# Optimization experiments

Hardware: AMD Instinct MI355X
Metric: run time of the kernel (lower is better)

Reference implementation:

```python
import jax, jax.numpy as jnp
import numpy as np

N = 32768      # total nodes per batched graph
E = 262144     # edges per batched graph (avg in-degree 8)
B = 64         # number of graphs in the batch (for mean_nodes readout)
DIN = 20
H = 512
BN_EPS = 1e-5


def setup_inputs() -> dict:
    key = jax.random.key(0)
    ks = jax.random.split(key, 24)
    p = lambda k, shape: jax.random.normal(k, shape, jnp.float32) * 0.02
    inp = {
        "x1": jax.random.normal(ks[0], (N, DIN), jnp.float32),
        "x2": jax.random.normal(ks[1], (N, DIN), jnp.float32),
        "src1": jax.random.randint(ks[2], (E,), 0, N, jnp.int32),
        "dst1": jax.random.randint(ks[3], (E,), 0, N, jnp.int32),
        "src2": jax.random.randint(ks[4], (E,), 0, N, jnp.int32),
        "dst2": jax.random.randint(ks[5], (E,), 0, N, jnp.int32),
        "gids1": jnp.repeat(jnp.arange(B, dtype=jnp.int32), N // B),
        "gids2": jnp.repeat(jnp.arange(B, dtype=jnp.int32), N // B),
        # shared parameters (applied to both graphs, as in the torch module)
        "W_init": p(ks[6], (DIN, H)), "b_init": jnp.zeros((H,), jnp.float32),
        "W1": p(ks[7], (H, H)), "b1": jnp.zeros((H,), jnp.float32),
        "W2": p(ks[8], (H, H)), "b2": jnp.zeros((H,), jnp.float32),
        "gamma1": jnp.ones((H,), jnp.float32), "beta1": jnp.zeros((H,), jnp.float32),
        "gamma2": jnp.ones((H,), jnp.float32), "beta2": jnp.zeros((H,), jnp.float32),
        "Wfc": p(ks[9], (2 * H, 256)), "bfc": jnp.zeros((256,), jnp.float32),
        "Wfc2": p(ks[10], (256, 1)), "bfc2": jnp.zeros((1,), jnp.float32),
    }
    return inp


def _bn_relu(z, gamma, beta):
    # BatchNorm1d in training mode: biased batch stats over the node axis
    mu = jnp.mean(z, axis=0)
    var = jnp.var(z, axis=0)
    return jax.nn.relu(gamma * (z - mu) * jax.lax.rsqrt(var + BN_EPS) + beta)


def _gin_mean(h, src, dst, W, b):
    # DGL GINConv(apply=Linear, aggregator='mean', eps=0):
    # out = Linear(h + mean_{j in N_in(v)} h_j); isolated nodes get 0 agg.
    msg_sum = jax.ops.segment_sum(h[src], dst, num_segments=N)      # [N,H]
    deg = jax.ops.segment_sum(jnp.ones((src.shape[0],), h.dtype), dst, num_segments=N)
    agg = msg_sum / jnp.maximum(deg, 1.0)[:, None]
    return (h + agg) @ W + b


def _encode(x, src, dst, gids, W_init, b_init, W1, b1, W2, b2,
            gamma1, beta1, gamma2, beta2):
    h0 = x @ W_init + b_init
    h1 = _bn_relu(_gin_mean(h0, src, dst, W1, b1), gamma1, beta1)
    h2 = _bn_relu(_gin_mean(h1, src, dst, W2, b2), gamma2, beta2)
    # dgl.mean_nodes: per-graph mean over nodes
    s = jax.ops.segment_sum(h2, gids, num_segments=B)               # [B,H]
    cnt = jax.ops.segment_sum(jnp.ones((h2.shape[0],), h2.dtype), gids, num_segments=B)
    return s / jnp.maximum(cnt, 1.0)[:, None]


def reference(x1, x2, src1, dst1, src2, dst2, gids1, gids2,
              W_init, b_init, W1, b1, W2, b2,
              gamma1, beta1, gamma2, beta2, Wfc, bfc, Wfc2, bfc2):
    g1_emb = _encode(x1, src1, dst1, gids1, W_init, b_init, W1, b1, W2, b2,
                     gamma1, beta1, gamma2, beta2)
    g2_emb = _encode(x2, src2, dst2, gids2, W_init, b_init, W1, b1, W2, b2,
                     gamma1, beta1, gamma2, beta2)
    x = jnp.concatenate([g1_emb, g2_emb], axis=1)                   # [B,2H]
    x = jax.nn.relu(x @ Wfc + bfc)
    return jax.nn.sigmoid(x @ Wfc2 + bfc2)                          # [B,1]
```

## Files before the change

kernel.cpp:

```cpp
#include <hip/hip_runtime.h>
#include <hip/hip_bf16.h>
#include <cstdint>

#define NN 32768
#define EE 262144
#define MM 65536
#define HH 512
#define BB 64
#define DIN 20
#define BN_EPS 1e-5f

__device__ __forceinline__ float bflo(uint32_t w) { return __builtin_bit_cast(float, w << 16); }
__device__ __forceinline__ float bfhi(uint32_t w) { return __builtin_bit_cast(float, w & 0xffff0000u); }
__device__ __forceinline__ uint32_t f2bf_u(float f) {
  uint32_t u = __builtin_bit_cast(uint32_t, f);
  return (u + 0x7fffu + ((u >> 16) & 1u)) >> 16;
}
__device__ __forceinline__ uint32_t pack2(float lo, float hi) {
  return f2bf_u(lo) | (f2bf_u(hi) << 16);
}

typedef float f32x4 __attribute__((ext_vector_type(4)));
typedef float f32x2 __attribute__((ext_vector_type(2)));

__device__ __forceinline__ void gl2lds16(const void* g, void* l) {
  __builtin_amdgcn_global_load_lds(
      (const __attribute__((address_space(1))) void*)g,
      (__attribute__((address_space(3))) void*)l, 16, 0, 0);
}

__global__ void prep_deg_kernel(const int* __restrict__ dst1, const int* __restrict__ dst2,
                                int* __restrict__ deg_cnt,
                                const float* __restrict__ W2, uint32_t* __restrict__ Wt8,
                                const float* __restrict__ Wi, const float* __restrict__ bi,
                                const float* __restrict__ W1, float* __restrict__ Wf) {
  int bid = blockIdx.x;
  if (bid < 2048) {
    int e = bid * 256 + threadIdx.x;
    int g = e >> 18, le = e & 0x3ffff;
    int d = (g ? dst2 : dst1)[le];
    atomicAdd(&deg_cnt[g * NN + d], 1);
  } else if (bid < 2304) {
    int idx = (bid - 2048) * 256 + threadIdx.x;
    int n = idx >> 7, k4 = idx & 127;
    int k = k4 * 4;
    float w0 = W2[(size_t)k * HH + n];
    float w1 = W2[(size_t)(k + 1) * HH + n];
    float w2v = W2[(size_t)(k + 2) * HH + n];
    float w3 = W2[(size_t)(k + 3) * HH + n];
    uint32_t p = __builtin_amdgcn_cvt_pk_fp8_f32(w0, w1, 0u, false);
    p = __builtin_amdgcn_cvt_pk_fp8_f32(w2v, w3, p, true);
    Wt8[(size_t)n * 128 + k4] = p;
  } else {
    int idx = (bid - 2304) * 256 + threadIdx.x;
    if (idx >= 21 * 512) return;
    int k = idx >> 9, n = idx & 511;
    float s = 0.f;
    if (k < 20) {
      const float* wr = Wi + (size_t)k * HH;
      for (int j = 0; j < HH; j++) s = fmaf(wr[j], W1[(size_t)j * HH + n], s);
    } else {
      for (int j = 0; j < HH; j++) s = fmaf(bi[j], W1[(size_t)j * HH + n], s);
    }
    Wf[idx] = s;
  }
}

__global__ void scan_kernel(const int* __restrict__ deg_cnt, int* __restrict__ offsets,
                            int* __restrict__ cursor) {
  int g = blockIdx.x;
  const int* d = deg_cnt + g * NN;
  int* off = offsets + g * (NN + 1);
  int* cur = cursor + g * NN;
  int t = threadIdx.x;
  int base = t * 32;
  int loc[32]; int s = 0;
#pragma unroll
  for (int i = 0; i < 32; i++) { loc[i] = d[base + i]; s += loc[i]; }
  __shared__ int sm[1024];
  sm[t] = s; __syncthreads();
  for (int ofs = 1; ofs < 1024; ofs <<= 1) {
    int v = sm[t];
    int add = (t >= ofs) ? sm[t - ofs] : 0;
    __syncthreads();
    sm[t] = v + add;
    __syncthreads();
  }
  int run = (t == 0) ? 0 : sm[t - 1];
#pragma unroll
  for (int i = 0; i < 32; i++) { off[base + i] = run; cur[base + i] = run; run += loc[i]; }
  if (t == 1023) off[NN] = run;
}

__global__ void scatter_kernel(const int* __restrict__ src1, const int* __restrict__ dst1,
                               const int* __restrict__ src2, const int* __restrict__ dst2,
                               int* __restrict__ cursor, int* __restrict__ csr) {
  int e = blockIdx.x * 256 + threadIdx.x;
  int g = e >> 18, le = e & 0x3ffff;
  int d = (g ? dst2 : dst1)[le];
  int s = (g ? src2 : src1)[le];
  int pos = atomicAdd(&cursor[g * NN + d], 1);
  csr[g * EE + pos] = s;
}

__global__ __launch_bounds__(256) void z1_kernel(const float* __restrict__ x1,
                          const float* __restrict__ x2,
                          const int* __restrict__ csr, const int* __restrict__ offsets,
                          const float* __restrict__ Wf, const float* __restrict__ b1,
                          uint16_t* __restrict__ z, uint32_t* __restrict__ z8,
                          float* __restrict__ pstat) {
  __shared__ float xas[128][21];
  int t = threadIdx.x;
  int r0 = blockIdx.x * 128;
  int g = r0 >> 15;
  const float* xg = g ? x2 : x1;
  const int* off = offsets + g * (NN + 1);
  const int* cs = csr + g * EE;

  {
    int row = t & 127;
    int half = t >> 7;
    int n = (r0 + row) & (NN - 1);
    int e0 = off[n], e1 = off[n + 1];
    int nf4 = half ? 2 : 3;
    int base4 = half ? 3 : 0;
    float4 a4[3] = {};
    for (int e = e0; e < e1; e++) {
      const float4* xr = (const float4*)(xg + (size_t)cs[e] * DIN) + base4;
      for (int k = 0; k < nf4; k++) {
        float4 v = xr[k];
        a4[k].x += v.x; a4[k].y += v.y; a4[k].z += v.z; a4[k].w += v.w;
      }
    }
    float inv = (e1 > e0) ? 1.f / (float)(e1 - e0) : 0.f;
    const float4* xs = (const float4*)(xg + (size_t)n * DIN) + base4;
    for (int k = 0; k < nf4; k++) {
      float4 v = xs[k];
      int d0 = (base4 + k) * 4;
      xas[row][d0 + 0] = fmaf(a4[k].x, inv, v.x);
      xas[row][d0 + 1] = fmaf(a4[k].y, inv, v.y);
      xas[row][d0 + 2] = fmaf(a4[k].z, inv, v.z);
      xas[row][d0 + 3] = fmaf(a4[k].w, inv, v.w);
    }
  }
  __syncthreads();

  int col0 = (t & 127) * 4;
  int rhalf = t >> 7;

  float w[DIN][4];
#pragma unroll
  for (int k = 0; k < DIN; k++) {
    float4 wv = *(const float4*)(Wf + (size_t)k * HH + col0);
    w[k][0] = wv.x; w[k][1] = wv.y; w[k][2] = wv.z; w[k][3] = wv.w;
  }
  float4 bvv = *(const float4*)(Wf + (size_t)DIN * HH + col0);
  float4 b1v = *(const float4*)(b1 + col0);

  float s4[4] = {0.f, 0.f, 0.f, 0.f}, q4[4] = {0.f, 0.f, 0.f, 0.f};
  for (int rr = 0; rr < 64; rr++) {
    int row = rr * 2 + rhalf;
    int grow = r0 + row;
    int n = grow & (NN - 1);
    float bf = (off[n + 1] - off[n] > 0) ? 2.f : 1.f;
    float a0 = fmaf(bvv.x, bf, b1v.x), a1 = fmaf(bvv.y, bf, b1v.y);
    float a2 = fmaf(bvv.z, bf, b1v.z), a3 = fmaf(bvv.w, bf, b1v.w);
#pragma unroll
    for (int k = 0; k < DIN; k++) {
      float xv = xas[row][k];
      a0 = fmaf(xv, w[k][0], a0);
      a1 = fmaf(xv, w[k][1], a1);
      a2 = fmaf(xv, w[k][2], a2);
      a3 = fmaf(xv, w[k][3], a3);
    }
    s4[0] += a0; q4[0] = fmaf(a0, a0, q4[0]);
    s4[1] += a1; q4[1] = fmaf(a1, a1, q4[1]);
    s4[2] += a2; q4[2] = fmaf(a2, a2, q4[2]);
    s4[3] += a3; q4[3] = fmaf(a3, a3, q4[3]);
    uint2 o;
    o.x = pack2(a0, a1); o.y = pack2(a2, a3);
    *(uint2*)(z + (size_t)grow * HH + col0) = o;
    uint32_t p8 = __builtin_amdgcn_cvt_pk_fp8_f32(a0, a1, 0u, false);
    p8 = __builtin_amdgcn_cvt_pk_fp8_f32(a2, a3, p8, true);
    z8[(size_t)grow * 128 + (col0 >> 2)] = p8;
  }

  __shared__ float sred[256][8];
#pragma unroll
  for (int k = 0; k < 4; k++) { sred[t][k] = s4[k]; sred[t][4 + k] = q4[k]; }
  __syncthreads();
  if (t < 128) {
    float* p = pstat + (size_t)blockIdx.x * 1024 + (size_t)col0 * 2;
#pragma unroll
    for (int k = 0; k < 4; k++) {
      p[k * 2 + 0] = sred[t][k] + sred[t + 128][k];
      p[k * 2 + 1] = sred[t][4 + k] + sred[t + 128][4 + k];
    }
  }
}

__global__ void reduce_stats(const float* __restrict__ pstat, const float* __restrict__ gamma,
                             const float* __restrict__ beta, float* __restrict__ scsh) {
  int b = blockIdx.x;
  int g = b >> 4, cg = b & 15;
  int t = threadIdx.x;
  int c = cg * 32 + (t & 31);
  int s = t >> 5;
  const float2* p = (const float2*)pstat + ((size_t)(g * 256 + s * 32)) * 512 + c;
  float sum = 0.f, q = 0.f;
  for (int m = 0; m < 32; m++) { float2 v = p[(size_t)m * 512]; sum += v.x; q += v.y; }
  __shared__ float ls[8][64];
  ls[s][(t & 31) * 2] = sum; ls[s][(t & 31) * 2 + 1] = q;
  __syncthreads();
  if (t < 32) {
    float S = 0.f, Q = 0.f;
#pragma unroll
    for (int k = 0; k < 8; k++) { S += ls[k][t * 2]; Q += ls[k][t * 2 + 1]; }
    int cc = cg * 32 + t;
    float mu = S * (1.f / (float)NN);
    float var = fmaxf(Q * (1.f / (float)NN) - mu * mu, 0.f);
    float sc = gamma[cc] * rsqrtf(var + BN_EPS);
    scsh[g * 1024 + cc * 2] = sc;
    scsh[g * 1024 + cc * 2 + 1] = beta[cc] - mu * sc;
  }
}

__device__ __forceinline__ void bn_acc8_fp8(uint2 v, const float* sc, const float* sh, float* acc) {
  f32x2 f01 = __builtin_amdgcn_cvt_pk_f32_fp8(v.x, false);
  f32x2 f23 = __builtin_amdgcn_cvt_pk_f32_fp8(v.x, true);
  f32x2 f45 = __builtin_amdgcn_cvt_pk_f32_fp8(v.y, false);
  f32x2 f67 = __builtin_amdgcn_cvt_pk_f32_fp8(v.y, true);
  acc[0] += fmaxf(fmaf(f01.x, sc[0], sh[0]), 0.f);
  acc[1] += fmaxf(fmaf(f01.y, sc[1], sh[1]), 0.f);
  acc[2] += fmaxf(fmaf(f23.x, sc[2], sh[2]), 0.f);
  acc[3] += fmaxf(fmaf(f23.y, sc[3], sh[3]), 0.f);
  acc[4] += fmaxf(fmaf(f45.x, sc[4], sh[4]), 0.f);
  acc[5] += fmaxf(fmaf(f45.y, sc[5], sh[5]), 0.f);
  acc[6] += fmaxf(fmaf(f67.x, sc[6], sh[6]), 0.f);
  acc[7] += fmaxf(fmaf(f67.y, sc[7], sh[7]), 0.f);
}

__global__ __launch_bounds__(256) void aggbn_kernel(const uint16_t* __restrict__ z,
                             const uint32_t* __restrict__ z8,
                             uint32_t* __restrict__ u8,
                             const int* __restrict__ csr, const int* __restrict__ offsets,
                             const float* __restrict__ scsh) {
  int wid = (blockIdx.x * 256 + threadIdx.x) >> 6;
  int lane = threadIdx.x & 63;
  int g = wid >> 15, n = wid & (NN - 1);
  const int* off = offsets + g * (NN + 1);
  int e0 = off[n], e1 = off[n + 1];
  const int* cs = csr + g * EE;
  const uint32_t* hb = (const uint32_t*)z;
  const uint32_t* base = hb + (size_t)g * NN * 256 + lane * 4;
  const uint32_t* base8 = z8 + (size_t)g * NN * 128 + lane * 2;

  uint4 hv = *(const uint4*)(base + (size_t)n * 256);

  const float4* ssp = (const float4*)(scsh + (size_t)g * HH * 2 + lane * 16);
  float4 ss0 = ssp[0], ss1 = ssp[1], ss2 = ssp[2], ss3 = ssp[3];
  float sc[8] = {ss0.x, ss0.z, ss1.x, ss1.z, ss2.x, ss2.z, ss3.x, ss3.z};
  float sh[8] = {ss0.y, ss0.w, ss1.y, ss1.w, ss2.y, ss2.w, ss3.y, ss3.w};
  float acc[8] = {0.f, 0.f, 0.f, 0.f, 0.f, 0.f, 0.f, 0.f};

  int e = e0;
  int rem = e1 - e0;
  int s0 = 0, s1 = 0, s2 = 0, s3 = 0;
  if (rem >= 4) { s0 = cs[e]; s1 = cs[e + 1]; s2 = cs[e + 2]; s3 = cs[e + 3]; }
  while (rem >= 4) {
    uint2 v0 = *(const uint2*)(base8 + (size_t)s0 * 128);
    uint2 v1 = *(const uint2*)(base8 + (size_t)s1 * 128);
    uint2 v2 = *(const uint2*)(base8 + (size_t)s2 * 128);
    uint2 v3 = *(const uint2*)(base8 + (size_t)s3 * 128);
    e += 4; rem -= 4;
    if (rem >= 4) { s0 = cs[e]; s1 = cs[e + 1]; s2 = cs[e + 2]; s3 = cs[e + 3]; }
    bn_acc8_fp8(v0, sc, sh, acc);
    bn_acc8_fp8(v1, sc, sh, acc);
    bn_acc8_fp8(v2, sc, sh, acc);
    bn_acc8_fp8(v3, sc, sh, acc);
  }
  for (; rem > 0; rem--, e++) {
    int s = cs[e];
    uint2 v = *(const uint2*)(base8 + (size_t)s * 128);
    bn_acc8_fp8(v, sc, sh, acc);
  }

  float inv = (e1 > e0) ? 1.f / (float)(e1 - e0) : 0.f;
  uint32_t wv[4] = {hv.x, hv.y, hv.z, hv.w};
  float o[8];
#pragma unroll
  for (int i = 0; i < 4; i++) {
    o[2 * i]     = fmaxf(fmaf(bflo(wv[i]), sc[2 * i],     sh[2 * i]),     0.f) + acc[2 * i] * inv;
    o[2 * i + 1] = fmaxf(fmaf(bfhi(wv[i]), sc[2 * i + 1], sh[2 * i + 1]), 0.f) + acc[2 * i + 1] * inv;
  }
  uint32_t q0 = __builtin_amdgcn_cvt_pk_fp8_f32(o[0], o[1], 0u, false);
  q0 = __builtin_amdgcn_cvt_pk_fp8_f32(o[2], o[3], q0, true);
  uint32_t q1 = __builtin_amdgcn_cvt_pk_fp8_f32(o[4], o[5], 0u, false);
  q1 = __builtin_amdgcn_cvt_pk_fp8_f32(o[6], o[7], q1, true);
  uint2 ov; ov.x = q0; ov.y = q1;
  *(uint2*)(u8 + (size_t)wid * 128 + lane * 2) = ov;
}

__global__ __launch_bounds__(256) void gemm_kernel(const uint8_t* __restrict__ A8,
                                                   const uint8_t* __restrict__ Bt8,
                                                   const float* __restrict__ bias,
                                                   uint16_t* __restrict__ C,
                                                   float* __restrict__ pstat) {
  __shared__ __align__(16) char lds[32768];
  uint8_t* sA = (uint8_t*)lds;
  uint8_t* sB = (uint8_t*)lds + 16384;
  const int tid = threadIdx.x;
  const int wave = tid >> 6;
  const int lane = tid & 63;
  const int bid = blockIdx.x;
  const int xcd = bid & 7;
  const int l = bid >> 3;
  const int nb = l & 3;
  const int mb = xcd * 64 + (l >> 2);
  const int m0 = mb * 128;
  const int n0 = nb * 128;
  const int fm = lane & 15;
  const int quad = lane >> 4;
  const int wr = wave >> 1, wc = wave & 1;

  const int sr = lane >> 3;
  const int slot = lane & 7;

  f32x4 acc[4][4] = {};
  for (int k0 = 0; k0 < HH; k0 += 128) {
    __syncthreads();
#pragma unroll
    for (int t = 0; t < 4; t++) {
      int R = t * 32 + wave * 8 + sr;
      int ksw = (slot ^ (R & 7)) * 16;
      gl2lds16(A8 + (size_t)(m0 + R) * HH + k0 + ksw, sA + R * 128 + slot * 16);
      gl2lds16(Bt8 + (size_t)(n0 + R) * HH + k0 + ksw, sB + R * 128 + slot * 16);
    }
    __syncthreads();
#pragma unroll
    for (int s2 = 0; s2 < 4; s2++) {
      const int k8 = s2 * 4 + quad;
      const int k16 = k8 >> 1;
      const int h8 = (k8 & 1) * 8;
      long a[4], b[4];
#pragma unroll
      for (int i = 0; i < 4; i++) {
        int r = wr * 64 + i * 16 + fm;
        a[i] = *(const long*)(sA + r * 128 + ((k16 ^ (r & 7)) * 16) + h8);
      }
#pragma unroll
      for (int j = 0; j < 4; j++) {
        int r = wc * 64 + j * 16 + fm;
        b[j] = *(const long*)(sB + r * 128 + ((k16 ^ (r & 7)) * 16) + h8);
      }
#pragma unroll
      for (int i = 0; i < 4; i++)
#pragma unroll
        for (int j = 0; j < 4; j++)
          acc[i][j] = __builtin_amdgcn_mfma_f32_16x16x32_fp8_fp8(a[i], b[j], acc[i][j], 0, 0, 0);
    }
  }

  float bj4[4];
#pragma unroll
  for (int j = 0; j < 4; j++) bj4[j] = bias[n0 + wc * 64 + j * 16 + fm];

  __syncthreads();
  float* ls = (float*)lds;
  if (tid < 256) ls[tid] = 0.f;
  __syncthreads();
#pragma unroll
  for (int j = 0; j < 4; j++) {
    int colloc = wc * 64 + j * 16 + fm;
    float sj = 0.f, qj = 0.f;
#pragma unroll
    for (int i = 0; i < 4; i++)
#pragma unroll
      for (int r = 0; r < 4; r++) {
        float f = acc[i][j][r] + bj4[j];
        sj += f; qj = fmaf(f, f, qj);
      }
    atomicAdd(&ls[colloc * 2], sj);
    atomicAdd(&ls[colloc * 2 + 1], qj);
  }
  __syncthreads();
  if (tid < 128) {
    float* p = pstat + (size_t)mb * 1024 + (size_t)(n0 + tid) * 2;
    p[0] = ls[tid * 2];
    p[1] = ls[tid * 2 + 1];
  }
  __syncthreads();

  uint16_t* sC = (uint16_t*)lds;
#pragma unroll
  for (int j = 0; j < 4; j++) {
    int col = wc * 64 + j * 16 + fm;
#pragma unroll
    for (int i = 0; i < 4; i++) {
      int rb = wr * 64 + i * 16 + quad * 4;
#pragma unroll
      for (int r = 0; r < 4; r++)
        sC[(rb + r) * 128 + col] = (uint16_t)f2bf_u(acc[i][j][r] + bj4[j]);
    }
  }
  __syncthreads();
  const int orow = tid >> 4;
  const int ocol = (tid & 15) * 8;
#pragma unroll
  for (int r8 = 0; r8 < 8; r8++) {
    int row = r8 * 16 + orow;
    uint4 v = *(const uint4*)(sC + row * 128 + ocol);
    *(uint4*)(C + (size_t)(m0 + row) * HH + n0 + ocol) = v;
  }
}

__global__ void bn2_readout(const uint16_t* __restrict__ z, const float* __restrict__ scsh,
                            const int* __restrict__ gids1, const int* __restrict__ gids2,
                            float* __restrict__ readout, float* __restrict__ cnt) {
  int blk = blockIdx.x;
  int r0 = blk * 128;
  int g = r0 >> 15;
  int lr = r0 & (NN - 1);
  int gid = (g ? gids2 : gids1)[lr];
  int t = threadIdx.x;
  int c = t * 2;
  const float* ss = scsh + (size_t)g * HH * 2;
  float sc0 = ss[c * 2], sh0 = ss[c * 2 + 1];
  float sc1 = ss[(c + 1) * 2], sh1 = ss[(c + 1) * 2 + 1];
  const uint32_t* p = (const uint32_t*)z + (size_t)r0 * 256 + t;
  float a0 = 0, a1 = 0;
  for (int r = 0; r < 128; r++) {
    uint32_t w = p[(size_t)r * 256];
    a0 += fmaxf(fmaf(bflo(w), sc0, sh0), 0.f);
    a1 += fmaxf(fmaf(bfhi(w), sc1, sh1), 0.f);
  }
  float* ro = readout + ((size_t)g * BB + gid) * HH;
  atomicAdd(&ro[c], a0);
  atomicAdd(&ro[c + 1], a1);
  if (t == 0) atomicAdd(&cnt[g * BB + gid], 128.f);
}

__global__ void final_kernel(const float* __restrict__ readout, const float* __restrict__ cnt,
                             const float* __restrict__ Wfc, const float* __restrict__ bfc,
                             const float* __restrict__ Wfc2, const float* __restrict__ bfc2,
                             float* __restrict__ out) {
  __shared__ float x[1024];
  __shared__ float red[256];
  int b = blockIdx.x, t = threadIdx.x;
  for (int i = t; i < 1024; i += 256) {
    int g = i >> 9, c = i & 511;
    float cc = cnt[g * BB + b];
    x[i] = readout[((size_t)g * BB + b) * HH + c] / fmaxf(cc, 1.f);
  }
  __syncthreads();
  float a0 = 0.f, a1 = 0.f, a2 = 0.f, a3 = 0.f;
  for (int i = 0; i < 1024; i += 4) {
    a0 = fmaf(x[i],     Wfc[(size_t)i * 256 + t],       a0);
    a1 = fmaf(x[i + 1], Wfc[(size_t)(i + 1) * 256 + t], a1);
    a2 = fmaf(x[i + 2], Wfc[(size_t)(i + 2) * 256 + t], a2);
    a3 = fmaf(x[i + 3], Wfc[(size_t)(i + 3) * 256 + t], a3);
  }
  float acc = bfc[t] + ((a0 + a1) + (a2 + a3));
  red[t] = fmaxf(acc, 0.f) * Wfc2[t];
  __syncthreads();
  for (int s = 128; s > 0; s >>= 1) {
    if (t < s) red[t] += red[t + s];
    __syncthreads();
  }
  if (t == 0) out[b] = 1.f / (1.f + expf(-(red[0] + bfc2[0])));
}

extern "C" void kernel_launch(void* const* d_in, const int* in_sizes, int n_in,
                              void* d_out, int out_size, void* d_ws, size_t ws_size,
                              hipStream_t stream) {
  const float* x1 = (const float*)d_in[0];
  const float* x2 = (const float*)d_in[1];
  const int* src1 = (const int*)d_in[2];
  const int* dst1 = (const int*)d_in[3];
  const int* src2 = (const int*)d_in[4];
  const int* dst2 = (const int*)d_in[5];
  const int* gids1 = (const int*)d_in[6];
  const int* gids2 = (const int*)d_in[7];
  const float* Wi = (const float*)d_in[8];
  const float* bi = (const float*)d_in[9];
  const float* W1 = (const float*)d_in[10];
  const float* b1 = (const float*)d_in[11];
  const float* W2 = (const float*)d_in[12];
  const float* b2 = (const float*)d_in[13];
  const float* gamma1 = (const float*)d_in[14];
  const float* beta1 = (const float*)d_in[15];
  const float* gamma2 = (const float*)d_in[16];
  const float* beta2 = (const float*)d_in[17];
  const float* Wfc = (const float*)d_in[18];
  const float* bfc = (const float*)d_in[19];
  const float* Wfc2 = (const float*)d_in[20];
  const float* bfc2 = (const float*)d_in[21];
  float* out = (float*)d_out;

  size_t off = 0;
  auto alloc = [&](size_t bytes) -> void* {
    void* p = (char*)d_ws + off;
    off += (bytes + 255) & ~(size_t)255;
    return p;
  };
  uint16_t* buf1 = (uint16_t*)alloc((size_t)MM * HH * 2);
  uint32_t* z8 = (uint32_t*)alloc((size_t)MM * HH);
  uint32_t* u8 = (uint32_t*)alloc((size_t)MM * HH);
  uint32_t* Wt8 = (uint32_t*)alloc((size_t)HH * HH);
  float* Wf = (float*)alloc((size_t)(DIN + 1) * HH * 4);
  int* csr = (int*)alloc((size_t)2 * EE * 4);
  int* offsets = (int*)alloc((size_t)2 * (NN + 1) * 4);
  int* cursor = (int*)alloc((size_t)2 * NN * 4);
  float* pbuf1 = (float*)alloc((size_t)512 * 512 * 2 * 4);
  float* pbuf2 = (float*)alloc((size_t)512 * 512 * 2 * 4);
  size_t zero_begin = off;
  int* deg_cnt = (int*)alloc((size_t)2 * NN * 4);
  float* readout = (float*)alloc((size_t)2 * BB * HH * 4);
  float* cnt = (float*)alloc((size_t)2 * BB * 4);
  size_t zero_end = off;
  float* scsh1 = (float*)alloc((size_t)2 * HH * 2 * 4);
  float* scsh2 = (float*)alloc((size_t)2 * HH * 2 * 4);
  (void)ws_size; (void)in_sizes; (void)n_in; (void)out_size;

  hipMemsetAsync((char*)d_ws + zero_begin, 0, zero_end - zero_begin, stream);

  prep_deg_kernel<<<2304 + 42, 256, 0, stream>>>(dst1, dst2, deg_cnt, W2, Wt8, Wi, bi, W1, Wf);
  scan_kernel<<<2, 1024, 0, stream>>>(deg_cnt, offsets, cursor);
  scatter_kernel<<<2048, 256, 0, stream>>>(src1, dst1, src2, dst2, cursor, csr);

  z1_kernel<<<MM / 128, 256, 0, stream>>>(x1, x2, csr, offsets, Wf, b1, buf1, z8, pbuf1);
  reduce_stats<<<32, 256, 0, stream>>>(pbuf1, gamma1, beta1, scsh1);

  aggbn_kernel<<<MM / 4, 256, 0, stream>>>(buf1, z8, u8, csr, offsets, scsh1);
  gemm_kernel<<<2048, 256, 0, stream>>>((const uint8_t*)u8, (const uint8_t*)Wt8, b2, buf1, pbuf2);
  reduce_stats<<<32, 256, 0, stream>>>(pbuf2, gamma2, beta2, scsh2);
  bn2_readout<<<MM / 128, 256, 0, stream>>>(buf1, scsh2, gids1, gids2, readout, cnt);

  final_kernel<<<BB, 256, 0, stream>>>(readout, cnt, Wfc, bfc, Wfc2, bfc2, out);
}
```

Before: 401.5 us.

## Drop bf16 z1 output and use fp8 self-term; split edge gather across 4 lanes

Result: faster. 369.9 us (-7.9%).

```diff
diff --git a/kernel.cpp b/kernel.cpp
--- a/kernel.cpp
+++ b/kernel.cpp
@@ -103,13 +103,13 @@
   csr[g * EE + pos] = s;
 }
 
-__global__ __launch_bounds__(256) void z1_kernel(const float* __restrict__ x1,
+__global__ __launch_bounds__(512) void z1_kernel(const float* __restrict__ x1,
                           const float* __restrict__ x2,
                           const int* __restrict__ csr, const int* __restrict__ offsets,
                           const float* __restrict__ Wf, const float* __restrict__ b1,
-                          uint16_t* __restrict__ z, uint32_t* __restrict__ z8,
-                          float* __restrict__ pstat) {
+                          uint32_t* __restrict__ z8, float* __restrict__ pstat) {
   __shared__ float xas[128][21];
+  __shared__ float sred[512][8];
   int t = threadIdx.x;
   int r0 = blockIdx.x * 128;
   int g = r0 >> 15;
@@ -118,35 +118,43 @@
   const int* cs = csr + g * EE;
 
   {
-    int row = t & 127;
-    int half = t >> 7;
+    int row = t >> 2;
+    int q = t & 3;
     int n = (r0 + row) & (NN - 1);
     int e0 = off[n], e1 = off[n + 1];
-    int nf4 = half ? 2 : 3;
-    int base4 = half ? 3 : 0;
-    float4 a4[3] = {};
-    for (int e = e0; e < e1; e++) {
-      const float4* xr = (const float4*)(xg + (size_t)cs[e] * DIN) + base4;
-      for (int k = 0; k < nf4; k++) {
+    float4 a4[5] = {};
+    for (int e = e0 + q; e < e1; e += 4) {
+      const float4* xr = (const float4*)(xg + (size_t)cs[e] * DIN);
+#pragma unroll
+      for (int k = 0; k < 5; k++) {
         float4 v = xr[k];
         a4[k].x += v.x; a4[k].y += v.y; a4[k].z += v.z; a4[k].w += v.w;
       }
     }
-    float inv = (e1 > e0) ? 1.f / (float)(e1 - e0) : 0.f;
-    const float4* xs = (const float4*)(xg + (size_t)n * DIN) + base4;
-    for (int k = 0; k < nf4; k++) {
-      float4 v = xs[k];
-      int d0 = (base4 + k) * 4;
-      xas[row][d0 + 0] = fmaf(a4[k].x, inv, v.x);
-      xas[row][d0 + 1] = fmaf(a4[k].y, inv, v.y);
-      xas[row][d0 + 2] = fmaf(a4[k].z, inv, v.z);
-      xas[row][d0 + 3] = fmaf(a4[k].w, inv, v.w);
+#pragma unroll
+    for (int k = 0; k < 5; k++) {
+      a4[k].x += __shfl_xor(a4[k].x, 1); a4[k].y += __shfl_xor(a4[k].y, 1);
+      a4[k].z += __shfl_xor(a4[k].z, 1); a4[k].w += __shfl_xor(a4[k].w, 1);
+      a4[k].x += __shfl_xor(a4[k].x, 2); a4[k].y += __shfl_xor(a4[k].y, 2);
+      a4[k].z += __shfl_xor(a4[k].z, 2); a4[k].w += __shfl_xor(a4[k].w, 2);
+    }
+    if (q == 0) {
+      float inv = (e1 > e0) ? 1.f / (float)(e1 - e0) : 0.f;
+      const float4* xs = (const float4*)(xg + (size_t)n * DIN);
+#pragma unroll
+      for (int k = 0; k < 5; k++) {
+        float4 v = xs[k];
+        xas[row][k * 4 + 0] = fmaf(a4[k].x, inv, v.x);
+        xas[row][k * 4 + 1] = fmaf(a4[k].y, inv, v.y);
+        xas[row][k * 4 + 2] = fmaf(a4[k].z, inv, v.z);
+        xas[row][k * 4 + 3] = fmaf(a4[k].w, inv, v.w);
+      }
     }
   }
   __syncthreads();
 
   int col0 = (t & 127) * 4;
-  int rhalf = t >> 7;
+  int rq = t >> 7;
 
   float w[DIN][4];
 #pragma unroll
@@ -158,8 +166,8 @@
   float4 b1v = *(const float4*)(b1 + col0);
 
   float s4[4] = {0.f, 0.f, 0.f, 0.f}, q4[4] = {0.f, 0.f, 0.f, 0.f};
-  for (int rr = 0; rr < 64; rr++) {
-    int row = rr * 2 + rhalf;
+  for (int rr = 0; rr < 32; rr++) {
+    int row = rr * 4 + rq;
     int grow = r0 + row;
     int n = grow & (NN - 1);
     float bf = (off[n + 1] - off[n] > 0) ? 2.f : 1.f;
@@ -177,15 +185,11 @@
     s4[1] += a1; q4[1] = fmaf(a1, a1, q4[1]);
     s4[2] += a2; q4[2] = fmaf(a2, a2, q4[2]);
     s4[3] += a3; q4[3] = fmaf(a3, a3, q4[3]);
-    uint2 o;
-    o.x = pack2(a0, a1); o.y = pack2(a2, a3);
-    *(uint2*)(z + (size_t)grow * HH + col0) = o;
     uint32_t p8 = __builtin_amdgcn_cvt_pk_fp8_f32(a0, a1, 0u, false);
     p8 = __builtin_amdgcn_cvt_pk_fp8_f32(a2, a3, p8, true);
     z8[(size_t)grow * 128 + (col0 >> 2)] = p8;
   }
 
-  __shared__ float sred[256][8];
 #pragma unroll
   for (int k = 0; k < 4; k++) { sred[t][k] = s4[k]; sred[t][4 + k] = q4[k]; }
   __syncthreads();
@@ -193,8 +197,8 @@
     float* p = pstat + (size_t)blockIdx.x * 1024 + (size_t)col0 * 2;
 #pragma unroll
     for (int k = 0; k < 4; k++) {
-      p[k * 2 + 0] = sred[t][k] + sred[t + 128][k];
-      p[k * 2 + 1] = sred[t][4 + k] + sred[t + 128][4 + k];
+      p[k * 2 + 0] = sred[t][k] + sred[t + 128][k] + sred[t + 256][k] + sred[t + 384][k];
+      p[k * 2 + 1] = sred[t][4 + k] + sred[t + 128][4 + k] + sred[t + 256][4 + k] + sred[t + 384][4 + k];
     }
   }
 }
@@ -240,8 +244,7 @@
   acc[7] += fmaxf(fmaf(f67.y, sc[7], sh[7]), 0.f);
 }
 
-__global__ __launch_bounds__(256) void aggbn_kernel(const uint16_t* __restrict__ z,
-                             const uint32_t* __restrict__ z8,
+__global__ __launch_bounds__(256) void aggbn_kernel(const uint32_t* __restrict__ z8,
                              uint32_t* __restrict__ u8,
                              const int* __restrict__ csr, const int* __restrict__ offsets,
                              const float* __restrict__ scsh) {
@@ -251,11 +254,9 @@
   const int* off = offsets + g * (NN + 1);
   int e0 = off[n], e1 = off[n + 1];
   const int* cs = csr + g * EE;
-  const uint32_t* hb = (const uint32_t*)z;
-  const uint32_t* base = hb + (size_t)g * NN * 256 + lane * 4;
   const uint32_t* base8 = z8 + (size_t)g * NN * 128 + lane * 2;
 
-  uint4 hv = *(const uint4*)(base + (size_t)n * 256);
+  uint2 hv8 = *(const uint2*)(base8 + (size_t)n * 128);
 
   const float4* ssp = (const float4*)(scsh + (size_t)g * HH * 2 + lane * 16);
   float4 ss0 = ssp[0], ss1 = ssp[1], ss2 = ssp[2], ss3 = ssp[3];
@@ -286,13 +287,15 @@
   }
 
   float inv = (e1 > e0) ? 1.f / (float)(e1 - e0) : 0.f;
-  uint32_t wv[4] = {hv.x, hv.y, hv.z, hv.w};
+  f32x2 h01 = __builtin_amdgcn_cvt_pk_f32_fp8(hv8.x, false);
+  f32x2 h23 = __builtin_amdgcn_cvt_pk_f32_fp8(hv8.x, true);
+  f32x2 h45 = __builtin_amdgcn_cvt_pk_f32_fp8(hv8.y, false);
+  f32x2 h67 = __builtin_amdgcn_cvt_pk_f32_fp8(hv8.y, true);
+  float hs[8] = {h01.x, h01.y, h23.x, h23.y, h45.x, h45.y, h67.x, h67.y};
   float o[8];
 #pragma unroll
-  for (int i = 0; i < 4; i++) {
-    o[2 * i]     = fmaxf(fmaf(bflo(wv[i]), sc[2 * i],     sh[2 * i]),     0.f) + acc[2 * i] * inv;
-    o[2 * i + 1] = fmaxf(fmaf(bfhi(wv[i]), sc[2 * i + 1], sh[2 * i + 1]), 0.f) + acc[2 * i + 1] * inv;
-  }
+  for (int i = 0; i < 8; i++)
+    o[i] = fmaxf(fmaf(hs[i], sc[i], sh[i]), 0.f) + acc[i] * inv;
   uint32_t q0 = __builtin_amdgcn_cvt_pk_fp8_f32(o[0], o[1], 0u, false);
   q0 = __builtin_amdgcn_cvt_pk_fp8_f32(o[2], o[3], q0, true);
   uint32_t q1 = __builtin_amdgcn_cvt_pk_fp8_f32(o[4], o[5], 0u, false);
@@ -528,10 +531,10 @@
   scan_kernel<<<2, 1024, 0, stream>>>(deg_cnt, offsets, cursor);
   scatter_kernel<<<2048, 256, 0, stream>>>(src1, dst1, src2, dst2, cursor, csr);
 
-  z1_kernel<<<MM / 128, 256, 0, stream>>>(x1, x2, csr, offsets, Wf, b1, buf1, z8, pbuf1);
+  z1_kernel<<<MM / 128, 512, 0, stream>>>(x1, x2, csr, offsets, Wf, b1, z8, pbuf1);
   reduce_stats<<<32, 256, 0, stream>>>(pbuf1, gamma1, beta1, scsh1);
 
-  aggbn_kernel<<<MM / 4, 256, 0, stream>>>(buf1, z8, u8, csr, offsets, scsh1);
+  aggbn_kernel<<<MM / 4, 256, 0, stream>>>(z8, u8, csr, offsets, scsh1);
   gemm_kernel<<<2048, 256, 0, stream>>>((const uint8_t*)u8, (const uint8_t*)Wt8, b2, buf1, pbuf2);
   reduce_stats<<<32, 256, 0, stream>>>(pbuf2, gamma2, beta2, scsh2);
   bn2_readout<<<MM / 128, 256, 0, stream>>>(buf1, scsh2, gids1, gids2, readout, cnt);
```
